# Kernel tuning notes

Measured on AMD Instinct MI355X. Metric: run time of the kernel, lower is better.

## Reference

```python
import jax, jax.numpy as jnp
import numpy as np

NUM_HEADS = 16
LN_EPS = 1e-5


def setup_inputs() -> dict:
    key = jax.random.key(0)
    ks = jax.random.split(key, 5)
    B, S, D = 2, 2048, 1024
    scale = 1.0 / np.sqrt(D)
    return {
        "x": jax.random.normal(ks[0], (B, S, D), dtype=jnp.float32),
        "in_proj_w": jax.random.normal(ks[1], (3 * D, D), dtype=jnp.float32) * scale,
        "in_proj_b": jnp.zeros((3 * D,), dtype=jnp.float32),
        "out_proj_w": jax.random.normal(ks[2], (D, D), dtype=jnp.float32) * scale,
        "out_proj_b": jnp.zeros((D,), dtype=jnp.float32),
        "ln_gamma": jnp.ones((D,), dtype=jnp.float32),
        "ln_beta": jnp.zeros((D,), dtype=jnp.float32),
    }


def reference(x, in_proj_w, in_proj_b, out_proj_w, out_proj_b, ln_gamma, ln_beta):
    # Faithful to nn.MultiheadAttention(batch_first=True, need_weights=True)
    # + residual + LayerNorm. Dropout is identity (eval mode).
    B, S, D = x.shape
    H = NUM_HEADS
    hd = D // H

    qkv = x @ in_proj_w.T + in_proj_b                      # [B,S,3D]
    q, k, v = jnp.split(qkv, 3, axis=-1)
    # [B,S,D] -> [B,H,S,hd]
    q = q.reshape(B, S, H, hd).transpose(0, 2, 1, 3)
    k = k.reshape(B, S, H, hd).transpose(0, 2, 1, 3)
    v = v.reshape(B, S, H, hd).transpose(0, 2, 1, 3)

    scores = jnp.einsum("bhqd,bhkd->bhqk", q, k) / jnp.sqrt(jnp.float32(hd))
    w = jax.nn.softmax(scores, axis=-1)                    # [B,H,S,S]
    ctx = jnp.einsum("bhqk,bhkd->bhqd", w, v)              # [B,H,S,hd]
    ctx = ctx.transpose(0, 2, 1, 3).reshape(B, S, D)
    attn_output = ctx @ out_proj_w.T + out_proj_b          # [B,S,D]

    # residual + LayerNorm (dropout disabled at inference)
    y = x + attn_output
    mu = jnp.mean(y, axis=-1, keepdims=True)
    var = jnp.var(y, axis=-1, keepdims=True)
    out = (y - mu) * jax.lax.rsqrt(var + LN_EPS) * ln_gamma + ln_beta

    # PyTorch default average_attn_weights=True -> mean over heads
    attn_weights = w.mean(axis=1)                          # [B,S,S]
    return (out, attn_weights)
```

## Files before the change

### kernel.cpp

```cpp
#include <hip/hip_runtime.h>
#include <math.h>

constexpr int B = 2, S = 2048, D = 1024, H = 16, HD = 64;
constexpr int T = B * S;
constexpr float EPS = 1e-5f;
constexpr float LOG2E = 1.44269504088896340736f;

typedef float f32x4 __attribute__((ext_vector_type(4)));
typedef __bf16 bf16x8 __attribute__((ext_vector_type(8)));
typedef unsigned short u16;

struct alignas(16) u4 { unsigned x, y, z, w; };
struct alignas(8) u2 { unsigned x, y; };

__device__ __forceinline__ u16 f2bf(float f) {
  union { __bf16 h; u16 u; } c;
  c.h = (__bf16)f;
  return c.u;
}
__device__ __forceinline__ float bf2f(u16 h) {
  return __uint_as_float(((unsigned)h) << 16);
}
__device__ __forceinline__ unsigned pk2(float a, float b) {
  return (unsigned)f2bf(a) | ((unsigned)f2bf(b) << 16);
}
__device__ __forceinline__ float fexp2(float x) {
  float r;
  asm("v_exp_f32 %0, %1" : "=v"(r) : "v"(x));
  return r;
}
__device__ __forceinline__ f32x4 MM(bf16x8 a, bf16x8 b, f32x4 c) {
  return __builtin_amdgcn_mfma_f32_16x16x32_bf16(a, b, c, 0, 0, 0);
}
union U16x8 { u4 q; bf16x8 b; };

__device__ __forceinline__ bf16x8 ld_frag(const u16* lds, int row, int chunk) {
  U16x8 u;
  u.q = *(const u4*)((const char*)lds + row * 128 + ((chunk ^ (row & 7)) * 16));
  return u.b;
}

template <int ITERS>
__device__ __forceinline__ void stageT(const u16* __restrict__ src, size_t off,
                                       int rstride, u16* lds, int tid) {
  const int lane = tid & 63, w = tid >> 6;
#pragma unroll
  for (int p = 0; p < ITERS; ++p) {
    const int idx = p * 256 + w * 64 + lane;
    const int r = idx >> 3, cc = idx & 7;
    const u16* gp = src + off + (size_t)r * rstride + ((cc ^ (r & 7)) * 8);
    u16* lp = lds + (size_t)(p * 256 + w * 64) * 8;
    __builtin_amdgcn_global_load_lds(
        (const __attribute__((address_space(1))) void*)gp,
        (__attribute__((address_space(3))) void*)lp, 16, 0, 0);
  }
}

__global__ __launch_bounds__(256) void k_split(const float* __restrict__ src,
                                               u16* __restrict__ hi,
                                               u16* __restrict__ lo, int n4) {
  const int i = blockIdx.x * 256 + threadIdx.x;
  if (i >= n4) return;
  const float4 v = ((const float4*)src)[i];
  u2 hh, ll;
  hh.x = pk2(v.x, v.y);
  hh.y = pk2(v.z, v.w);
  ll.x = pk2(v.x - bf2f((u16)hh.x), v.y - bf2f((u16)(hh.x >> 16)));
  ll.y = pk2(v.z - bf2f((u16)hh.y), v.w - bf2f((u16)(hh.y >> 16)));
  ((u2*)hi)[i] = hh;
  ((u2*)lo)[i] = ll;
}

__global__ __launch_bounds__(256, 2) void k_qkv(
    const u16* __restrict__ xh, const u16* __restrict__ xl,
    const u16* __restrict__ wh, const u16* __restrict__ wl,
    const float* __restrict__ bias, u16* __restrict__ Qh, u16* __restrict__ Ql,
    u16* __restrict__ Kh, u16* __restrict__ Kl, u16* __restrict__ Vh,
    u16* __restrict__ Vl) {
  __shared__ u16 Ah[8192], Al[8192], Bh[8192], Bl[8192];
  const int tid = threadIdx.x;
  const int w = tid >> 6, lane = tid & 63;
  const int j = lane & 15, g = lane >> 4;
  const int wr = w >> 1, wc = w & 1;
  const int row0 = blockIdx.y * 128;
  const int col0 = blockIdx.x * 128;
  const f32x4 z4 = {0.f, 0.f, 0.f, 0.f};
  f32x4 acc[4][4];
#pragma unroll
  for (int mi = 0; mi < 4; ++mi)
#pragma unroll
    for (int ni = 0; ni < 4; ++ni) acc[mi][ni] = z4;

  for (int k0 = 0; k0 < D; k0 += 64) {
    __syncthreads();
    stageT<4>(xh, (size_t)row0 * D + k0, D, Ah, tid);
    stageT<4>(xl, (size_t)row0 * D + k0, D, Al, tid);
    stageT<4>(wh, (size_t)col0 * D + k0, D, Bh, tid);
    stageT<4>(wl, (size_t)col0 * D + k0, D, Bl, tid);
    __syncthreads();
#pragma unroll
    for (int kk = 0; kk < 2; ++kk) {
      bf16x8 afh[4], afl[4], bfh[4], bfl[4];
#pragma unroll
      for (int mi = 0; mi < 4; ++mi) {
        afh[mi] = ld_frag(Ah, wr * 64 + 16 * mi + j, kk * 4 + g);
        afl[mi] = ld_frag(Al, wr * 64 + 16 * mi + j, kk * 4 + g);
      }
#pragma unroll
      for (int ni = 0; ni < 4; ++ni) {
        bfh[ni] = ld_frag(Bh, wc * 64 + 16 * ni + j, kk * 4 + g);
        bfl[ni] = ld_frag(Bl, wc * 64 + 16 * ni + j, kk * 4 + g);
      }
#pragma unroll
      for (int mi = 0; mi < 4; ++mi)
#pragma unroll
        for (int ni = 0; ni < 4; ++ni) {
          acc[mi][ni] = MM(afh[mi], bfh[ni], acc[mi][ni]);
          acc[mi][ni] = MM(afh[mi], bfl[ni], acc[mi][ni]);
          acc[mi][ni] = MM(afl[mi], bfh[ni], acc[mi][ni]);
        }
    }
  }

  const int part = col0 >> 10;
  if (part < 2) {
    const float qsc = (part == 0) ? 0.125f * LOG2E : 1.0f;
    u16* dh = (part == 0) ? Qh : Kh;
    u16* dl = (part == 0) ? Ql : Kl;
#pragma unroll
    for (int ni = 0; ni < 4; ++ni) {
      const int col = col0 + wc * 64 + 16 * ni + j;
      const int h = (col & 1023) >> 6, hd = col & 63;
      const float bv = bias[col];
#pragma unroll
      for (int mi = 0; mi < 4; ++mi)
#pragma unroll
        for (int r = 0; r < 4; ++r) {
          const int tok = row0 + wr * 64 + 16 * mi + 4 * g + r;
          const int bb = tok >> 11, ss = tok & 2047;
          const float v = (acc[mi][ni][r] + bv) * qsc;
          const size_t o = (((size_t)bb * H + h) * S + ss) * HD + hd;
          const u16 hv = f2bf(v);
          dh[o] = hv;
          dl[o] = f2bf(v - bf2f(hv));
        }
    }
  } else {
#pragma unroll
    for (int ni = 0; ni < 4; ++ni) {
      const int col = col0 + wc * 64 + 16 * ni + j;
      const int h = (col & 1023) >> 6, hd = col & 63;
      const float bv = bias[col];
#pragma unroll
      for (int mi = 0; mi < 4; ++mi) {
        const int tok0 = row0 + wr * 64 + 16 * mi + 4 * g;
        const int bb = tok0 >> 11, ss = tok0 & 2047;
        const float v0 = acc[mi][ni][0] + bv, v1 = acc[mi][ni][1] + bv;
        const float v2 = acc[mi][ni][2] + bv, v3 = acc[mi][ni][3] + bv;
        const u16 h0 = f2bf(v0), h1 = f2bf(v1), h2 = f2bf(v2), h3 = f2bf(v3);
        const size_t o = (((size_t)bb * H + h) * HD + hd) * S + ss;
        u2 ph, pl;
        ph.x = (unsigned)h0 | ((unsigned)h1 << 16);
        ph.y = (unsigned)h2 | ((unsigned)h3 << 16);
        pl.x = pk2(v0 - bf2f(h0), v1 - bf2f(h1));
        pl.y = pk2(v2 - bf2f(h2), v3 - bf2f(h3));
        *(u2*)(Vh + o) = ph;
        *(u2*)(Vl + o) = pl;
      }
    }
  }
}

__global__ __launch_bounds__(256, 2) void k_ctx(
    const u16* __restrict__ Qh, const u16* __restrict__ Ql,
    const u16* __restrict__ Kh, const u16* __restrict__ Kl,
    const u16* __restrict__ Vh, const u16* __restrict__ Vl,
    u16* __restrict__ ch, u16* __restrict__ cl, float* __restrict__ mo,
    float* __restrict__ lo) {
  __shared__ u16 Ksh[4096], Ksl[4096], Vsh[4096], Vsl[4096];
  const int tid = threadIdx.x;
  const int w = tid >> 6, lane = tid & 63;
  const int j = lane & 15, g = lane >> 4;
  const int q0 = blockIdx.x * 128;
  const int h = blockIdx.y, b = blockIdx.z;
  const size_t hb = (size_t)b * H + h;
  int qr[2];
  qr[0] = q0 + 32 * w + j;
  qr[1] = qr[0] + 16;

  bf16x8 qfh[2][2], qfl[2][2];
#pragma unroll
  for (int s = 0; s < 2; ++s)
#pragma unroll
    for (int kk = 0; kk < 2; ++kk) {
      const size_t o = (hb * S + qr[s]) * HD + kk * 32 + 8 * g;
      U16x8 u;
      u.q = *(const u4*)(Qh + o);
      qfh[s][kk] = u.b;
      u.q = *(const u4*)(Ql + o);
      qfl[s][kk] = u.b;
    }

  const f32x4 z4 = {0.f, 0.f, 0.f, 0.f};
  f32x4 ctxa[2][4];
#pragma unroll
  for (int s = 0; s < 2; ++s)
#pragma unroll
    for (int mf = 0; mf < 4; ++mf) ctxa[s][mf] = z4;
  float m_run[2] = {-INFINITY, -INFINITY};
  float l_run[2] = {0.f, 0.f};

  for (int k0 = 0; k0 < S; k0 += 64) {
    __syncthreads();
    stageT<2>(Kh, (hb * S + k0) * HD, HD, Ksh, tid);
    stageT<2>(Kl, (hb * S + k0) * HD, HD, Ksl, tid);
    stageT<2>(Vh, hb * HD * S + k0, S, Vsh, tid);
    stageT<2>(Vl, hb * HD * S + k0, S, Vsl, tid);
    __syncthreads();

    f32x4 st[2][4];
#pragma unroll
    for (int s = 0; s < 2; ++s)
#pragma unroll
      for (int kb = 0; kb < 4; ++kb) st[s][kb] = z4;
#pragma unroll
    for (int kk = 0; kk < 2; ++kk) {
      bf16x8 kh4[4], kl4[4];
#pragma unroll
      for (int kb = 0; kb < 4; ++kb) {
        kh4[kb] = ld_frag(Ksh, 16 * kb + j, kk * 4 + g);
        kl4[kb] = ld_frag(Ksl, 16 * kb + j, kk * 4 + g);
      }
#pragma unroll
      for (int s = 0; s < 2; ++s)
#pragma unroll
        for (int kb = 0; kb < 4; ++kb) {
          st[s][kb] = MM(kh4[kb], qfh[s][kk], st[s][kb]);
          st[s][kb] = MM(kh4[kb], qfl[s][kk], st[s][kb]);
          st[s][kb] = MM(kl4[kb], qfh[s][kk], st[s][kb]);
        }
    }

    U16x8 pbh[2][2], pbl[2][2];
#pragma unroll
    for (int s = 0; s < 2; ++s) {
      float pm = -INFINITY;
#pragma unroll
      for (int kb = 0; kb < 4; ++kb)
#pragma unroll
        for (int r = 0; r < 4; ++r) pm = fmaxf(pm, st[s][kb][r]);
      pm = fmaxf(pm, __shfl_xor(pm, 16));
      pm = fmaxf(pm, __shfl_xor(pm, 32));
      const float m_new = fmaxf(m_run[s], pm);
      const float sc = fexp2(m_run[s] - m_new);
      m_run[s] = m_new;
      float p[4][4];
      float ls = 0.f;
#pragma unroll
      for (int kb = 0; kb < 4; ++kb)
#pragma unroll
        for (int r = 0; r < 4; ++r) {
          p[kb][r] = fexp2(st[s][kb][r] - m_new);
          ls += p[kb][r];
        }
      l_run[s] = l_run[s] * sc + ls;
#pragma unroll
      for (int mf = 0; mf < 4; ++mf) ctxa[s][mf] *= sc;

      unsigned ph[4][2], pl[4][2];
#pragma unroll
      for (int kb = 0; kb < 4; ++kb) {
        const u16 a0 = f2bf(p[kb][0]), a1 = f2bf(p[kb][1]);
        const u16 a2 = f2bf(p[kb][2]), a3 = f2bf(p[kb][3]);
        ph[kb][0] = (unsigned)a0 | ((unsigned)a1 << 16);
        ph[kb][1] = (unsigned)a2 | ((unsigned)a3 << 16);
        pl[kb][0] = pk2(p[kb][0] - bf2f(a0), p[kb][1] - bf2f(a1));
        pl[kb][1] = pk2(p[kb][2] - bf2f(a2), p[kb][3] - bf2f(a3));
      }
      const int srcA = ((g & 1) << 5) + j;
      const int srcB = srcA + 16;
      const bool hikb = (g >> 1) != 0;
#pragma unroll
      for (int t = 0; t < 2; ++t) {
        const unsigned w0a = __shfl(ph[2 * t][0], srcA),
                       w0b = __shfl(ph[2 * t + 1][0], srcA);
        const unsigned w1a = __shfl(ph[2 * t][1], srcA),
                       w1b = __shfl(ph[2 * t + 1][1], srcA);
        const unsigned w2a = __shfl(ph[2 * t][0], srcB),
                       w2b = __shfl(ph[2 * t + 1][0], srcB);
        const unsigned w3a = __shfl(ph[2 * t][1], srcB),
                       w3b = __shfl(ph[2 * t + 1][1], srcB);
        pbh[s][t].q.x = hikb ? w0b : w0a;
        pbh[s][t].q.y = hikb ? w1b : w1a;
        pbh[s][t].q.z = hikb ? w2b : w2a;
        pbh[s][t].q.w = hikb ? w3b : w3a;
        const unsigned v0a = __shfl(pl[2 * t][0], srcA),
                       v0b = __shfl(pl[2 * t + 1][0], srcA);
        const unsigned v1a = __shfl(pl[2 * t][1], srcA),
                       v1b = __shfl(pl[2 * t + 1][1], srcA);
        const unsigned v2a = __shfl(pl[2 * t][0], srcB),
                       v2b = __shfl(pl[2 * t + 1][0], srcB);
        const unsigned v3a = __shfl(pl[2 * t][1], srcB),
                       v3b = __shfl(pl[2 * t + 1][1], srcB);
        pbl[s][t].q.x = hikb ? v0b : v0a;
        pbl[s][t].q.y = hikb ? v1b : v1a;
        pbl[s][t].q.z = hikb ? v2b : v2a;
        pbl[s][t].q.w = hikb ? v3b : v3a;
      }
    }

#pragma unroll
    for (int t = 0; t < 2; ++t)
#pragma unroll
      for (int mf = 0; mf < 4; ++mf) {
        const bf16x8 vh_ = ld_frag(Vsh, 16 * mf + j, t * 4 + g);
        const bf16x8 vl_ = ld_frag(Vsl, 16 * mf + j, t * 4 + g);
#pragma unroll
        for (int s = 0; s < 2; ++s) {
          ctxa[s][mf] = MM(vh_, pbh[s][t].b, ctxa[s][mf]);
          ctxa[s][mf] = MM(vh_, pbl[s][t].b, ctxa[s][mf]);
          ctxa[s][mf] = MM(vl_, pbh[s][t].b, ctxa[s][mf]);
        }
      }
  }

#pragma unroll
  for (int s = 0; s < 2; ++s) {
    float lt = l_run[s];
    lt += __shfl_xor(lt, 16);
    lt += __shfl_xor(lt, 32);
    const float inv = 1.0f / lt;
    const int tokg = b * S + qr[s];
#pragma unroll
    for (int mf = 0; mf < 4; ++mf) {
      const int feat = h * HD + 16 * mf + 4 * g;
      const float v0 = ctxa[s][mf][0] * inv, v1 = ctxa[s][mf][1] * inv;
      const float v2 = ctxa[s][mf][2] * inv, v3 = ctxa[s][mf][3] * inv;
      const u16 h0 = f2bf(v0), h1 = f2bf(v1), h2 = f2bf(v2), h3 = f2bf(v3);
      const size_t o = (size_t)tokg * D + feat;
      u2 hh, ll;
      hh.x = (unsigned)h0 | ((unsigned)h1 << 16);
      hh.y = (unsigned)h2 | ((unsigned)h3 << 16);
      ll.x = pk2(v0 - bf2f(h0), v1 - bf2f(h1));
      ll.y = pk2(v2 - bf2f(h2), v3 - bf2f(h3));
      *(u2*)(ch + o) = hh;
      *(u2*)(cl + o) = ll;
    }
    if (g == 0) {
      mo[hb * S + qr[s]] = m_run[s];
      lo[hb * S + qr[s]] = inv;
    }
  }
}

__global__ __launch_bounds__(256, 2) void k_oproj(
    const u16* __restrict__ ah_, const u16* __restrict__ al_,
    const u16* __restrict__ wh, const u16* __restrict__ wl,
    const float* __restrict__ bias, const float* __restrict__ x,
    float* __restrict__ y) {
  __shared__ u16 Ah[8192], Al[8192], Bh[8192], Bl[8192];
  const int tid = threadIdx.x;
  const int w = tid >> 6, lane = tid & 63;
  const int j = lane & 15, g = lane >> 4;
  const int wr = w >> 1, wc = w & 1;
  const int row0 = blockIdx.y * 128;
  const int col0 = blockIdx.x * 128;
  const f32x4 z4 = {0.f, 0.f, 0.f, 0.f};
  f32x4 acc[4][4];
#pragma unroll
  for (int mi = 0; mi < 4; ++mi)
#pragma unroll
    for (int ni = 0; ni < 4; ++ni) acc[mi][ni] = z4;

  for (int k0 = 0; k0 < D; k0 += 64) {
    __syncthreads();
    stageT<4>(ah_, (size_t)row0 * D + k0, D, Ah, tid);
    stageT<4>(al_, (size_t)row0 * D + k0, D, Al, tid);
    stageT<4>(wh, (size_t)col0 * D + k0, D, Bh, tid);
    stageT<4>(wl, (size_t)col0 * D + k0, D, Bl, tid);
    __syncthreads();
#pragma unroll
    for (int kk = 0; kk < 2; ++kk) {
      bf16x8 afh[4], afl[4], bfh[4], bfl[4];
#pragma unroll
      for (int mi = 0; mi < 4; ++mi) {
        afh[mi] = ld_frag(Ah, wr * 64 + 16 * mi + j, kk * 4 + g);
        afl[mi] = ld_frag(Al, wr * 64 + 16 * mi + j, kk * 4 + g);
      }
#pragma unroll
      for (int ni = 0; ni < 4; ++ni) {
        bfh[ni] = ld_frag(Bh, wc * 64 + 16 * ni + j, kk * 4 + g);
        bfl[ni] = ld_frag(Bl, wc * 64 + 16 * ni + j, kk * 4 + g);
      }
#pragma unroll
      for (int mi = 0; mi < 4; ++mi)
#pragma unroll
        for (int ni = 0; ni < 4; ++ni) {
          acc[mi][ni] = MM(afh[mi], bfh[ni], acc[mi][ni]);
          acc[mi][ni] = MM(afh[mi], bfl[ni], acc[mi][ni]);
          acc[mi][ni] = MM(afl[mi], bfh[ni], acc[mi][ni]);
        }
    }
  }
#pragma unroll
  for (int ni = 0; ni < 4; ++ni) {
    const int col = col0 + wc * 64 + 16 * ni + j;
    const float bv = bias[col];
#pragma unroll
    for (int mi = 0; mi < 4; ++mi)
#pragma unroll
      for (int r = 0; r < 4; ++r) {
        const int tok = row0 + wr * 64 + 16 * mi + 4 * g + r;
        const size_t off = (size_t)tok * D + col;
        y[off] = acc[mi][ni][r] + bv + x[off];
      }
  }
}

__global__ __launch_bounds__(256, 2) void k_wts(
    const u16* __restrict__ Qh, const u16* __restrict__ Ql,
    const u16* __restrict__ Kh, const u16* __restrict__ Kl,
    const float* __restrict__ mi, const float* __restrict__ li,
    float* __restrict__ attn) {
  __shared__ u16 Ksh[4096], Ksl[4096];
  const int tid = threadIdx.x;
  const int w = tid >> 6, lane = tid & 63;
  const int j = lane & 15, g = lane >> 4;
  const int k0 = blockIdx.x * 64;
  const int q0 = blockIdx.y * 128;
  const int b = blockIdx.z;
  const f32x4 z4 = {0.f, 0.f, 0.f, 0.f};
  f32x4 wacc[2][4];
#pragma unroll
  for (int s = 0; s < 2; ++s)
#pragma unroll
    for (int nf = 0; nf < 4; ++nf) wacc[s][nf] = z4;

  for (int h = 0; h < H; ++h) {
    const size_t hb = (size_t)b * H + h;
    __syncthreads();
    stageT<2>(Kh, (hb * S + k0) * HD, HD, Ksh, tid);
    stageT<2>(Kl, (hb * S + k0) * HD, HD, Ksl, tid);
    __syncthreads();
    bf16x8 qfh[2][2], qfl[2][2];
#pragma unroll
    for (int s = 0; s < 2; ++s)
#pragma unroll
      for (int kk = 0; kk < 2; ++kk) {
        const size_t o = (hb * S + q0 + 32 * w + 16 * s + j) * HD + kk * 32 + 8 * g;
        U16x8 u;
        u.q = *(const u4*)(Qh + o);
        qfh[s][kk] = u.b;
        u.q = *(const u4*)(Ql + o);
        qfl[s][kk] = u.b;
      }
    f32x4 sacc[2][4];
#pragma unroll
    for (int s = 0; s < 2; ++s)
#pragma unroll
      for (int nf = 0; nf < 4; ++nf) sacc[s][nf] = z4;
#pragma unroll
    for (int kk = 0; kk < 2; ++kk) {
#pragma unroll
      for (int nf = 0; nf < 4; ++nf) {
        const bf16x8 kh_ = ld_frag(Ksh, 16 * nf + j, kk * 4 + g);
        const bf16x8 kl_ = ld_frag(Ksl, 16 * nf + j, kk * 4 + g);
#pragma unroll
        for (int s = 0; s < 2; ++s) {
          sacc[s][nf] = MM(qfh[s][kk], kh_, sacc[s][nf]);
          sacc[s][nf] = MM(qfh[s][kk], kl_, sacc[s][nf]);
          sacc[s][nf] = MM(qfl[s][kk], kh_, sacc[s][nf]);
        }
      }
    }
#pragma unroll
    for (int s = 0; s < 2; ++s)
#pragma unroll
      for (int r = 0; r < 4; ++r) {
        const size_t o = hb * S + q0 + 32 * w + 16 * s + 4 * g + r;
        const float m = mi[o];
        const float lv = li[o];
#pragma unroll
        for (int nf = 0; nf < 4; ++nf)
          wacc[s][nf][r] = fmaf(fexp2(sacc[s][nf][r] - m), lv, wacc[s][nf][r]);
      }
  }
  const float ih = 1.0f / (float)H;
#pragma unroll
  for (int s = 0; s < 2; ++s)
#pragma unroll
    for (int nf = 0; nf < 4; ++nf)
#pragma unroll
      for (int r = 0; r < 4; ++r) {
        const size_t row = (size_t)b * S + q0 + 32 * w + 16 * s + 4 * g + r;
        attn[row * S + k0 + 16 * nf + j] = wacc[s][nf][r] * ih;
      }
}

__global__ __launch_bounds__(256) void k_ln(float* __restrict__ y,
                                            const float* __restrict__ gamma,
                                            const float* __restrict__ beta) {
  const int row = blockIdx.x;
  const int tid = threadIdx.x;
  const float4 v = *reinterpret_cast<const float4*>(&y[(size_t)row * D + tid * 4]);
  float s = v.x + v.y + v.z + v.w;
  float sq = v.x * v.x + v.y * v.y + v.z * v.z + v.w * v.w;
#pragma unroll
  for (int off = 32; off > 0; off >>= 1) {
    s += __shfl_down(s, off);
    sq += __shfl_down(sq, off);
  }
  __shared__ float sm[8];
  const int wid = tid >> 6, lane = tid & 63;
  if (lane == 0) {
    sm[wid] = s;
    sm[4 + wid] = sq;
  }
  __syncthreads();
  s = sm[0] + sm[1] + sm[2] + sm[3];
  sq = sm[4] + sm[5] + sm[6] + sm[7];
  const float mu = s * (1.0f / D);
  const float var = sq * (1.0f / D) - mu * mu;
  const float rstd = rsqrtf(var + EPS);
  const float4 gmv = *reinterpret_cast<const float4*>(&gamma[tid * 4]);
  const float4 btv = *reinterpret_cast<const float4*>(&beta[tid * 4]);
  float4 o;
  o.x = (v.x - mu) * rstd * gmv.x + btv.x;
  o.y = (v.y - mu) * rstd * gmv.y + btv.y;
  o.z = (v.z - mu) * rstd * gmv.z + btv.z;
  o.w = (v.w - mu) * rstd * gmv.w + btv.w;
  *reinterpret_cast<float4*>(&y[(size_t)row * D + tid * 4]) = o;
}

extern "C" void kernel_launch(void* const* d_in, const int* in_sizes, int n_in,
                              void* d_out, int out_size, void* d_ws,
                              size_t ws_size, hipStream_t stream) {
  const float* x = (const float*)d_in[0];
  const float* inW = (const float*)d_in[1];
  const float* inB = (const float*)d_in[2];
  const float* outW = (const float*)d_in[3];
  const float* outB = (const float*)d_in[4];
  const float* gamma = (const float*)d_in[5];
  const float* beta = (const float*)d_in[6];

  float* out = (float*)d_out;
  float* attn = out + (size_t)T * D;

  char* ab = (char*)attn;
  u16* xh = (u16*)(ab);
  u16* xl = (u16*)(ab + (8u << 20));
  u16* wih = (u16*)(ab + (16u << 20));
  u16* wil = (u16*)(ab + (22u << 20));
  u16* woh = (u16*)(ab + (28u << 20));
  u16* wol = (u16*)(ab + (30u << 20));
  u16* cth = xh;
  u16* ctl = xl;

  char* wsb = (char*)d_ws;
  u16* Qh = (u16*)(wsb);
  u16* Ql = (u16*)(wsb + (8u << 20));
  u16* Kh = (u16*)(wsb + (16u << 20));
  u16* Kl = (u16*)(wsb + (24u << 20));
  u16* Vh = (u16*)(wsb + (32u << 20));
  u16* Vl = (u16*)(wsb + (40u << 20));
  float* mo = (float*)(wsb + (48u << 20));
  float* lo = (float*)(wsb + (48u << 20) + 262144);

  k_split<<<4096, 256, 0, stream>>>(x, xh, xl, T * D / 4);
  k_split<<<3072, 256, 0, stream>>>(inW, wih, wil, 3 * D * D / 4);
  k_split<<<1024, 256, 0, stream>>>(outW, woh, wol, D * D / 4);
  k_qkv<<<dim3(24, 32), 256, 0, stream>>>(xh, xl, wih, wil, inB, Qh, Ql, Kh,
                                          Kl, Vh, Vl);
  k_ctx<<<dim3(16, 16, 2), 256, 0, stream>>>(Qh, Ql, Kh, Kl, Vh, Vl, cth, ctl,
                                             mo, lo);
  k_oproj<<<dim3(8, 32), 256, 0, stream>>>(cth, ctl, woh, wol, outB, x, out);
  k_wts<<<dim3(32, 16, 2), 256, 0, stream>>>(Qh, Ql, Kh, Kl, mo, lo, attn);
  k_ln<<<T, 256, 0, stream>>>(out, gamma, beta);
}
```

Before: 458.9 us.

## Double-buffer LDS staging in the GEMM, attention-context and weights kernels

Each main loop now issues the async global-to-LDS loads for the next tile into a second buffer before computing on the current one, and keeps a single barrier at the end of each iteration. The aim is to hide global load latency behind MFMA work. The QKV and output GEMMs drop the K tile from 64 to 32 so total LDS stays the same, which doubles their iteration and barrier count. The ctx and wts kernels double their LDS footprint, which could limit how many blocks fit per CU.

```diff
diff --git a/kernel.cpp b/kernel.cpp
--- a/kernel.cpp
+++ b/kernel.cpp
@@ -39,7 +39,6 @@
   u.q = *(const u4*)((const char*)lds + row * 128 + ((chunk ^ (row & 7)) * 16));
   return u.b;
 }
-
 template <int ITERS>
 __device__ __forceinline__ void stageT(const u16* __restrict__ src, size_t off,
                                        int rstride, u16* lds, int tid) {
@@ -49,6 +48,27 @@
     const int idx = p * 256 + w * 64 + lane;
     const int r = idx >> 3, cc = idx & 7;
     const u16* gp = src + off + (size_t)r * rstride + ((cc ^ (r & 7)) * 8);
+    u16* lp = lds + (size_t)(p * 256 + w * 64) * 8;
+    __builtin_amdgcn_global_load_lds(
+        (const __attribute__((address_space(1))) void*)gp,
+        (__attribute__((address_space(3))) void*)lp, 16, 0, 0);
+  }
+}
+
+__device__ __forceinline__ bf16x8 ld_frag32(const u16* lds, int row, int chunk) {
+  U16x8 u;
+  u.q = *(const u4*)((const char*)lds + row * 64 + ((chunk ^ (row & 3)) * 16));
+  return u.b;
+}
+template <int ITERS>
+__device__ __forceinline__ void stage32(const u16* __restrict__ src, size_t off,
+                                        int rstride, u16* lds, int tid) {
+  const int lane = tid & 63, w = tid >> 6;
+#pragma unroll
+  for (int p = 0; p < ITERS; ++p) {
+    const int idx = p * 256 + w * 64 + lane;
+    const int r = idx >> 2, cc = idx & 3;
+    const u16* gp = src + off + (size_t)r * rstride + ((cc ^ (r & 3)) * 8);
     u16* lp = lds + (size_t)(p * 256 + w * 64) * 8;
     __builtin_amdgcn_global_load_lds(
         (const __attribute__((address_space(1))) void*)gp,
@@ -77,7 +97,7 @@
     const float* __restrict__ bias, u16* __restrict__ Qh, u16* __restrict__ Ql,
     u16* __restrict__ Kh, u16* __restrict__ Kl, u16* __restrict__ Vh,
     u16* __restrict__ Vl) {
-  __shared__ u16 Ah[8192], Al[8192], Bh[8192], Bl[8192];
+  __shared__ u16 Ah[2][4096], Al[2][4096], Bh[2][4096], Bl[2][4096];
   const int tid = threadIdx.x;
   const int w = tid >> 6, lane = tid & 63;
   const int j = lane & 15, g = lane >> 4;
@@ -91,35 +111,41 @@
 #pragma unroll
     for (int ni = 0; ni < 4; ++ni) acc[mi][ni] = z4;
 
-  for (int k0 = 0; k0 < D; k0 += 64) {
+  stage32<2>(xh, (size_t)row0 * D, D, Ah[0], tid);
+  stage32<2>(xl, (size_t)row0 * D, D, Al[0], tid);
+  stage32<2>(wh, (size_t)col0 * D, D, Bh[0], tid);
+  stage32<2>(wl, (size_t)col0 * D, D, Bl[0], tid);
+  __syncthreads();
+
+  for (int t = 0; t < 32; ++t) {
+    const int cur = t & 1;
+    if (t < 31) {
+      const int k0 = (t + 1) * 32;
+      stage32<2>(xh, (size_t)row0 * D + k0, D, Ah[cur ^ 1], tid);
+      stage32<2>(xl, (size_t)row0 * D + k0, D, Al[cur ^ 1], tid);
+      stage32<2>(wh, (size_t)col0 * D + k0, D, Bh[cur ^ 1], tid);
+      stage32<2>(wl, (size_t)col0 * D + k0, D, Bl[cur ^ 1], tid);
+    }
+    bf16x8 afh[4], afl[4], bfh[4], bfl[4];
+#pragma unroll
+    for (int mi = 0; mi < 4; ++mi) {
+      afh[mi] = ld_frag32(Ah[cur], wr * 64 + 16 * mi + j, g);
+      afl[mi] = ld_frag32(Al[cur], wr * 64 + 16 * mi + j, g);
+    }
+#pragma unroll
+    for (int ni = 0; ni < 4; ++ni) {
+      bfh[ni] = ld_frag32(Bh[cur], wc * 64 + 16 * ni + j, g);
+      bfl[ni] = ld_frag32(Bl[cur], wc * 64 + 16 * ni + j, g);
+    }
+#pragma unroll
+    for (int mi = 0; mi < 4; ++mi)
+#pragma unroll
+      for (int ni = 0; ni < 4; ++ni) {
+        acc[mi][ni] = MM(afh[mi], bfh[ni], acc[mi][ni]);
+        acc[mi][ni] = MM(afh[mi], bfl[ni], acc[mi][ni]);
+        acc[mi][ni] = MM(afl[mi], bfh[ni], acc[mi][ni]);
+      }
     __syncthreads();
-    stageT<4>(xh, (size_t)row0 * D + k0, D, Ah, tid);
-    stageT<4>(xl, (size_t)row0 * D + k0, D, Al, tid);
-    stageT<4>(wh, (size_t)col0 * D + k0, D, Bh, tid);
-    stageT<4>(wl, (size_t)col0 * D + k0, D, Bl, tid);
-    __syncthreads();
-#pragma unroll
-    for (int kk = 0; kk < 2; ++kk) {
-      bf16x8 afh[4], afl[4], bfh[4], bfl[4];
-#pragma unroll
-      for (int mi = 0; mi < 4; ++mi) {
-        afh[mi] = ld_frag(Ah, wr * 64 + 16 * mi + j, kk * 4 + g);
-        afl[mi] = ld_frag(Al, wr * 64 + 16 * mi + j, kk * 4 + g);
-      }
-#pragma unroll
-      for (int ni = 0; ni < 4; ++ni) {
-        bfh[ni] = ld_frag(Bh, wc * 64 + 16 * ni + j, kk * 4 + g);
-        bfl[ni] = ld_frag(Bl, wc * 64 + 16 * ni + j, kk * 4 + g);
-      }
-#pragma unroll
-      for (int mi = 0; mi < 4; ++mi)
-#pragma unroll
-        for (int ni = 0; ni < 4; ++ni) {
-          acc[mi][ni] = MM(afh[mi], bfh[ni], acc[mi][ni]);
-          acc[mi][ni] = MM(afh[mi], bfl[ni], acc[mi][ni]);
-          acc[mi][ni] = MM(afl[mi], bfh[ni], acc[mi][ni]);
-        }
-    }
   }
 
   const int part = col0 >> 10;
@@ -177,7 +203,7 @@
     const u16* __restrict__ Vh, const u16* __restrict__ Vl,
     u16* __restrict__ ch, u16* __restrict__ cl, float* __restrict__ mo,
     float* __restrict__ lo) {
-  __shared__ u16 Ksh[4096], Ksl[4096], Vsh[4096], Vsl[4096];
+  __shared__ u16 Ksh[2][4096], Ksl[2][4096], Vsh[2][4096], Vsl[2][4096];
   const int tid = threadIdx.x;
   const int w = tid >> 6, lane = tid & 63;
   const int j = lane & 15, g = lane >> 4;
@@ -210,13 +236,21 @@
   float m_run[2] = {-INFINITY, -INFINITY};
   float l_run[2] = {0.f, 0.f};
 
-  for (int k0 = 0; k0 < S; k0 += 64) {
-    __syncthreads();
-    stageT<2>(Kh, (hb * S + k0) * HD, HD, Ksh, tid);
-    stageT<2>(Kl, (hb * S + k0) * HD, HD, Ksl, tid);
-    stageT<2>(Vh, hb * HD * S + k0, S, Vsh, tid);
-    stageT<2>(Vl, hb * HD * S + k0, S, Vsl, tid);
-    __syncthreads();
+  stageT<2>(Kh, hb * S * HD, HD, Ksh[0], tid);
+  stageT<2>(Kl, hb * S * HD, HD, Ksl[0], tid);
+  stageT<2>(Vh, hb * HD * S, S, Vsh[0], tid);
+  stageT<2>(Vl, hb * HD * S, S, Vsl[0], tid);
+  __syncthreads();
+
+  for (int t = 0; t < 32; ++t) {
+    const int cur = t & 1;
+    if (t < 31) {
+      const int k0 = (t + 1) * 64;
+      stageT<2>(Kh, (hb * S + k0) * HD, HD, Ksh[cur ^ 1], tid);
+      stageT<2>(Kl, (hb * S + k0) * HD, HD, Ksl[cur ^ 1], tid);
+      stageT<2>(Vh, hb * HD * S + k0, S, Vsh[cur ^ 1], tid);
+      stageT<2>(Vl, hb * HD * S + k0, S, Vsl[cur ^ 1], tid);
+    }
 
     f32x4 st[2][4];
 #pragma unroll
@@ -228,8 +262,8 @@
       bf16x8 kh4[4], kl4[4];
 #pragma unroll
       for (int kb = 0; kb < 4; ++kb) {
-        kh4[kb] = ld_frag(Ksh, 16 * kb + j, kk * 4 + g);
-        kl4[kb] = ld_frag(Ksl, 16 * kb + j, kk * 4 + g);
+        kh4[kb] = ld_frag(Ksh[cur], 16 * kb + j, kk * 4 + g);
+        kl4[kb] = ld_frag(Ksl[cur], 16 * kb + j, kk * 4 + g);
       }
 #pragma unroll
       for (int s = 0; s < 2; ++s)
@@ -281,47 +315,48 @@
       const int srcB = srcA + 16;
       const bool hikb = (g >> 1) != 0;
 #pragma unroll
-      for (int t = 0; t < 2; ++t) {
-        const unsigned w0a = __shfl(ph[2 * t][0], srcA),
-                       w0b = __shfl(ph[2 * t + 1][0], srcA);
-        const unsigned w1a = __shfl(ph[2 * t][1], srcA),
-                       w1b = __shfl(ph[2 * t + 1][1], srcA);
-        const unsigned w2a = __shfl(ph[2 * t][0], srcB),
-                       w2b = __shfl(ph[2 * t + 1][0], srcB);
-        const unsigned w3a = __shfl(ph[2 * t][1], srcB),
-                       w3b = __shfl(ph[2 * t + 1][1], srcB);
-        pbh[s][t].q.x = hikb ? w0b : w0a;
-        pbh[s][t].q.y = hikb ? w1b : w1a;
-        pbh[s][t].q.z = hikb ? w2b : w2a;
-        pbh[s][t].q.w = hikb ? w3b : w3a;
-        const unsigned v0a = __shfl(pl[2 * t][0], srcA),
-                       v0b = __shfl(pl[2 * t + 1][0], srcA);
-        const unsigned v1a = __shfl(pl[2 * t][1], srcA),
-                       v1b = __shfl(pl[2 * t + 1][1], srcA);
-        const unsigned v2a = __shfl(pl[2 * t][0], srcB),
-                       v2b = __shfl(pl[2 * t + 1][0], srcB);
-        const unsigned v3a = __shfl(pl[2 * t][1], srcB),
-                       v3b = __shfl(pl[2 * t + 1][1], srcB);
-        pbl[s][t].q.x = hikb ? v0b : v0a;
-        pbl[s][t].q.y = hikb ? v1b : v1a;
-        pbl[s][t].q.z = hikb ? v2b : v2a;
-        pbl[s][t].q.w = hikb ? v3b : v3a;
-      }
-    }
-
-#pragma unroll
-    for (int t = 0; t < 2; ++t)
+      for (int t2 = 0; t2 < 2; ++t2) {
+        const unsigned w0a = __shfl(ph[2 * t2][0], srcA),
+                       w0b = __shfl(ph[2 * t2 + 1][0], srcA);
+        const unsigned w1a = __shfl(ph[2 * t2][1], srcA),
+                       w1b = __shfl(ph[2 * t2 + 1][1], srcA);
+        const unsigned w2a = __shfl(ph[2 * t2][0], srcB),
+                       w2b = __shfl(ph[2 * t2 + 1][0], srcB);
+        const unsigned w3a = __shfl(ph[2 * t2][1], srcB),
+                       w3b = __shfl(ph[2 * t2 + 1][1], srcB);
+        pbh[s][t2].q.x = hikb ? w0b : w0a;
+        pbh[s][t2].q.y = hikb ? w1b : w1a;
+        pbh[s][t2].q.z = hikb ? w2b : w2a;
+        pbh[s][t2].q.w = hikb ? w3b : w3a;
+        const unsigned v0a = __shfl(pl[2 * t2][0], srcA),
+                       v0b = __shfl(pl[2 * t2 + 1][0], srcA);
+        const unsigned v1a = __shfl(pl[2 * t2][1], srcA),
+                       v1b = __shfl(pl[2 * t2 + 1][1], srcA);
+        const unsigned v2a = __shfl(pl[2 * t2][0], srcB),
+                       v2b = __shfl(pl[2 * t2 + 1][0], srcB);
+        const unsigned v3a = __shfl(pl[2 * t2][1], srcB),
+                       v3b = __shfl(pl[2 * t2 + 1][1], srcB);
+        pbl[s][t2].q.x = hikb ? v0b : v0a;
+        pbl[s][t2].q.y = hikb ? v1b : v1a;
+        pbl[s][t2].q.z = hikb ? v2b : v2a;
+        pbl[s][t2].q.w = hikb ? v3b : v3a;
+      }
+    }
+
+#pragma unroll
+    for (int t2 = 0; t2 < 2; ++t2)
 #pragma unroll
       for (int mf = 0; mf < 4; ++mf) {
-        const bf16x8 vh_ = ld_frag(Vsh, 16 * mf + j, t * 4 + g);
-        const bf16x8 vl_ = ld_frag(Vsl, 16 * mf + j, t * 4 + g);
+        const bf16x8 vh_ = ld_frag(Vsh[cur], 16 * mf + j, t2 * 4 + g);
+        const bf16x8 vl_ = ld_frag(Vsl[cur], 16 * mf + j, t2 * 4 + g);
 #pragma unroll
         for (int s = 0; s < 2; ++s) {
-          ctxa[s][mf] = MM(vh_, pbh[s][t].b, ctxa[s][mf]);
-          ctxa[s][mf] = MM(vh_, pbl[s][t].b, ctxa[s][mf]);
-          ctxa[s][mf] = MM(vl_, pbh[s][t].b, ctxa[s][mf]);
+          ctxa[s][mf] = MM(vh_, pbh[s][t2].b, ctxa[s][mf]);
+          ctxa[s][mf] = MM(vh_, pbl[s][t2].b, ctxa[s][mf]);
+          ctxa[s][mf] = MM(vl_, pbh[s][t2].b, ctxa[s][mf]);
         }
       }
+    __syncthreads();
   }
 
 #pragma unroll
@@ -358,7 +393,7 @@
     const u16* __restrict__ wh, const u16* __restrict__ wl,
     const float* __restrict__ bias, const float* __restrict__ x,
     float* __restrict__ y) {
-  __shared__ u16 Ah[8192], Al[8192], Bh[8192], Bl[8192];
+  __shared__ u16 Ah[2][4096], Al[2][4096], Bh[2][4096], Bl[2][4096];
   const int tid = threadIdx.x;
   const int w = tid >> 6, lane = tid & 63;
   const int j = lane & 15, g = lane >> 4;
@@ -372,35 +407,41 @@
 #pragma unroll
     for (int ni = 0; ni < 4; ++ni) acc[mi][ni] = z4;
 
-  for (int k0 = 0; k0 < D; k0 += 64) {
+  stage32<2>(ah_, (size_t)row0 * D, D, Ah[0], tid);
+  stage32<2>(al_, (size_t)row0 * D, D, Al[0], tid);
+  stage32<2>(wh, (size_t)col0 * D, D, Bh[0], tid);
+  stage32<2>(wl, (size_t)col0 * D, D, Bl[0], tid);
+  __syncthreads();
+
+  for (int t = 0; t < 32; ++t) {
+    const int cur = t & 1;
+    if (t < 31) {
+      const int k0 = (t + 1) * 32;
+      stage32<2>(ah_, (size_t)row0 * D + k0, D, Ah[cur ^ 1], tid);
+      stage32<2>(al_, (size_t)row0 * D + k0, D, Al[cur ^ 1], tid);
+      stage32<2>(wh, (size_t)col0 * D + k0, D, Bh[cur ^ 1], tid);
+      stage32<2>(wl, (size_t)col0 * D + k0, D, Bl[cur ^ 1], tid);
+    }
+    bf16x8 afh[4], afl[4], bfh[4], bfl[4];
+#pragma unroll
+    for (int mi = 0; mi < 4; ++mi) {
+      afh[mi] = ld_frag32(Ah[cur], wr * 64 + 16 * mi + j, g);
+      afl[mi] = ld_frag32(Al[cur], wr * 64 + 16 * mi + j, g);
+    }
+#pragma unroll
+    for (int ni = 0; ni < 4; ++ni) {
+      bfh[ni] = ld_frag32(Bh[cur], wc * 64 + 16 * ni + j, g);
+      bfl[ni] = ld_frag32(Bl[cur], wc * 64 + 16 * ni + j, g);
+    }
+#pragma unroll
+    for (int mi = 0; mi < 4; ++mi)
+#pragma unroll
+      for (int ni = 0; ni < 4; ++ni) {
+        acc[mi][ni] = MM(afh[mi], bfh[ni], acc[mi][ni]);
+        acc[mi][ni] = MM(afh[mi], bfl[ni], acc[mi][ni]);
+        acc[mi][ni] = MM(afl[mi], bfh[ni], acc[mi][ni]);
+      }
     __syncthreads();
-    stageT<4>(ah_, (size_t)row0 * D + k0, D, Ah, tid);
-    stageT<4>(al_, (size_t)row0 * D + k0, D, Al, tid);
-    stageT<4>(wh, (size_t)col0 * D + k0, D, Bh, tid);
-    stageT<4>(wl, (size_t)col0 * D + k0, D, Bl, tid);
-    __syncthreads();
-#pragma unroll
-    for (int kk = 0; kk < 2; ++kk) {
-      bf16x8 afh[4], afl[4], bfh[4], bfl[4];
-#pragma unroll
-      for (int mi = 0; mi < 4; ++mi) {
-        afh[mi] = ld_frag(Ah, wr * 64 + 16 * mi + j, kk * 4 + g);
-        afl[mi] = ld_frag(Al, wr * 64 + 16 * mi + j, kk * 4 + g);
-      }
-#pragma unroll
-      for (int ni = 0; ni < 4; ++ni) {
-        bfh[ni] = ld_frag(Bh, wc * 64 + 16 * ni + j, kk * 4 + g);
-        bfl[ni] = ld_frag(Bl, wc * 64 + 16 * ni + j, kk * 4 + g);
-      }
-#pragma unroll
-      for (int mi = 0; mi < 4; ++mi)
-#pragma unroll
-        for (int ni = 0; ni < 4; ++ni) {
-          acc[mi][ni] = MM(afh[mi], bfh[ni], acc[mi][ni]);
-          acc[mi][ni] = MM(afh[mi], bfl[ni], acc[mi][ni]);
-          acc[mi][ni] = MM(afl[mi], bfh[ni], acc[mi][ni]);
-        }
-    }
   }
 #pragma unroll
   for (int ni = 0; ni < 4; ++ni) {
@@ -422,7 +463,7 @@
     const u16* __restrict__ Kh, const u16* __restrict__ Kl,
     const float* __restrict__ mi, const float* __restrict__ li,
     float* __restrict__ attn) {
-  __shared__ u16 Ksh[4096], Ksl[4096];
+  __shared__ u16 Ksh[2][4096], Ksl[2][4096];
   const int tid = threadIdx.x;
   const int w = tid >> 6, lane = tid & 63;
   const int j = lane & 15, g = lane >> 4;
@@ -436,12 +477,21 @@
 #pragma unroll
     for (int nf = 0; nf < 4; ++nf) wacc[s][nf] = z4;
 
+  {
+    const size_t hb0 = (size_t)b * H;
+    stageT<2>(Kh, (hb0 * S + k0) * HD, HD, Ksh[0], tid);
+    stageT<2>(Kl, (hb0 * S + k0) * HD, HD, Ksl[0], tid);
+  }
+  __syncthreads();
+
   for (int h = 0; h < H; ++h) {
+    const int cur = h & 1;
     const size_t hb = (size_t)b * H + h;
-    __syncthreads();
-    stageT<2>(Kh, (hb * S + k0) * HD, HD, Ksh, tid);
-    stageT<2>(Kl, (hb * S + k0) * HD, HD, Ksl, tid);
-    __syncthreads();
+    if (h < H - 1) {
+      const size_t hbn = hb + 1;
+      stageT<2>(Kh, (hbn * S + k0) * HD, HD, Ksh[cur ^ 1], tid);
+      stageT<2>(Kl, (hbn * S + k0) * HD, HD, Ksl[cur ^ 1], tid);
+    }
     bf16x8 qfh[2][2], qfl[2][2];
 #pragma unroll
     for (int s = 0; s < 2; ++s)
@@ -463,8 +513,8 @@
     for (int kk = 0; kk < 2; ++kk) {
 #pragma unroll
       for (int nf = 0; nf < 4; ++nf) {
-        const bf16x8 kh_ = ld_frag(Ksh, 16 * nf + j, kk * 4 + g);
-        const bf16x8 kl_ = ld_frag(Ksl, 16 * nf + j, kk * 4 + g);
+        const bf16x8 kh_ = ld_frag(Ksh[cur], 16 * nf + j, kk * 4 + g);
+        const bf16x8 kl_ = ld_frag(Ksl[cur], 16 * nf + j, kk * 4 + g);
 #pragma unroll
         for (int s = 0; s < 2; ++s) {
           sacc[s][nf] = MM(qfh[s][kk], kh_, sacc[s][nf]);
@@ -484,6 +534,7 @@
         for (int nf = 0; nf < 4; ++nf)
           wacc[s][nf][r] = fmaf(fexp2(sacc[s][nf][r] - m), lv, wacc[s][nf][r]);
       }
+    __syncthreads();
   }
   const float ih = 1.0f / (float)H;
 #pragma unroll
```

New measurement: 492.4 us. 1.07x slower.
